# Kernel optimization log

Hardware: AMD Instinct MI355X
Metric: run time of the kernel (lower is better)

## Reference

```python
import jax, jax.numpy as jnp
import numpy as np

B, K, D = 4, 8192, 1024


def setup_inputs() -> dict:
    key = jax.random.key(0)
    kx, kw, kb = jax.random.split(key, 3)
    x = jax.random.normal(kx, (B, K, D), dtype=jnp.float32)
    # torch.nn.Linear default init: U(-1/sqrt(fan_in), 1/sqrt(fan_in))
    bound = 1.0 / np.sqrt(D)
    W = jax.random.uniform(kw, (D, D), dtype=jnp.float32, minval=-bound, maxval=bound)
    b = jax.random.uniform(kb, (D,), dtype=jnp.float32, minval=-bound, maxval=bound)
    return {"x": x, "W": W, "b": b}


def reference(x, W, b):
    # lam_t = sigmoid(x_t @ W^T + b): compute for all timesteps in one GEMM
    lam = jax.nn.sigmoid(jnp.einsum("bkd,ed->bke", x, W) + b)  # [B,K,D]
    u_gated = (1.0 - lam) * x  # [B,K,D]

    def step(s, inputs):
        lam_t, ug_t = inputs  # each [B,D]
        s = lam_t * s + ug_t
        return s, s

    s0 = jnp.zeros((x.shape[0], x.shape[2]), dtype=x.dtype)
    # scan over time axis: move K to leading dim
    _, ys = jax.lax.scan(step, s0, (jnp.swapaxes(lam, 0, 1), jnp.swapaxes(u_gated, 0, 1)))
    return jnp.swapaxes(ys, 0, 1)  # [B,K,D]
```

## Files before the change

kernel.cpp:

```cpp
#include <hip/hip_runtime.h>
#include <hip/hip_bf16.h>
#include <hip/hip_fp16.h>
#include <cstdint>
#include <cstddef>

#define B_ 4
#define K_ 8192
#define D_ 1024
#define M_ (B_*K_)
#define BD_ (B_*D_)

#define CCH 256
#define LCH (K_/CCH)

typedef __bf16    bf16x8 __attribute__((ext_vector_type(8)));
typedef float     f32x4  __attribute__((ext_vector_type(4)));
typedef _Float16  f16x4  __attribute__((ext_vector_type(4)));

typedef __attribute__((address_space(1))) void as1void;
typedef __attribute__((address_space(3))) void as3void;

__device__ __forceinline__ void gload_lds16(const void* g, void* l) {
  __builtin_amdgcn_global_load_lds((as1void*)g, (as3void*)l, 16, 0, 0);
}

__device__ __forceinline__ unsigned short f2bf_rne(float f) {
  unsigned u = __builtin_bit_cast(unsigned, f);
  u += 0x7fffu + ((u >> 16) & 1u);
  return (unsigned short)(u >> 16);
}

__global__ __launch_bounds__(256) void cvt_f32_to_bf16(
    const float* __restrict__ in, unsigned short* __restrict__ out, int n4) {
  int stride = gridDim.x * blockDim.x;
  for (int i = blockIdx.x * blockDim.x + threadIdx.x; i < n4; i += stride) {
    float4 v = reinterpret_cast<const float4*>(in)[i];
    ushort4 o;
    o.x = f2bf_rne(v.x); o.y = f2bf_rne(v.y);
    o.z = f2bf_rne(v.z); o.w = f2bf_rne(v.w);
    reinterpret_cast<ushort4*>(out)[i] = o;
  }
}

__global__ __launch_bounds__(256) void gemm_bias_sigmoid(
    const unsigned short* __restrict__ A,
    const unsigned short* __restrict__ Bw,
    const float* __restrict__ bias,
    _Float16* __restrict__ lamh) {
  __shared__ __attribute__((aligned(16))) unsigned short Alds[128 * 32];
  __shared__ __attribute__((aligned(16))) unsigned short Blds[128 * 32];

  const int t    = threadIdx.x;
  const int wave = t >> 6;
  const int lane = t & 63;
  const int wr   = wave >> 1;
  const int wc   = wave & 1;
  const int m0   = blockIdx.x * 128;
  const int n0   = blockIdx.y * 128;

  f32x4 acc[4][4] = {};

  const int r0 = t >> 2;
  const int c0 = (t & 3) * 8;
  const unsigned short* gA0 = A  + (size_t)(m0 + r0)      * D_ + c0;
  const unsigned short* gA1 = A  + (size_t)(m0 + r0 + 64) * D_ + c0;
  const unsigned short* gB0 = Bw + (size_t)(n0 + r0)      * D_ + c0;
  const unsigned short* gB1 = Bw + (size_t)(n0 + r0 + 64) * D_ + c0;
  unsigned short* lA0 = Alds + (       wave * 64) * 8;
  unsigned short* lA1 = Alds + (256 +  wave * 64) * 8;
  unsigned short* lB0 = Blds + (       wave * 64) * 8;
  unsigned short* lB1 = Blds + (256 +  wave * 64) * 8;

  const int aoff = (wr * 64 + (lane & 15)) * 32 + ((lane >> 4) * 8);
  const int boff = (wc * 64 + (lane & 15)) * 32 + ((lane >> 4) * 8);

  for (int kt = 0; kt < D_; kt += 32) {
    gload_lds16(gA0 + kt, lA0);
    gload_lds16(gA1 + kt, lA1);
    gload_lds16(gB0 + kt, lB0);
    gload_lds16(gB1 + kt, lB1);
    __syncthreads();
    bf16x8 af[4], bf[4];
#pragma unroll
    for (int m = 0; m < 4; ++m)
      af[m] = *reinterpret_cast<const bf16x8*>(&Alds[aoff + m * 16 * 32]);
#pragma unroll
    for (int n = 0; n < 4; ++n)
      bf[n] = *reinterpret_cast<const bf16x8*>(&Blds[boff + n * 16 * 32]);
#pragma unroll
    for (int m = 0; m < 4; ++m)
#pragma unroll
      for (int n = 0; n < 4; ++n)
        acc[m][n] = __builtin_amdgcn_mfma_f32_16x16x32_bf16(af[m], bf[n], acc[m][n], 0, 0, 0);
    __syncthreads();
  }

  const int erow = m0 + wr * 64 + ((lane >> 4) << 2);
  const int ecol = n0 + wc * 64 + (lane & 15);
#pragma unroll
  for (int n = 0; n < 4; ++n) {
    const int col = ecol + n * 16;
    const float bv = bias[col];
#pragma unroll
    for (int m = 0; m < 4; ++m) {
#pragma unroll
      for (int r = 0; r < 4; ++r) {
        const int row = erow + m * 16 + r;
        const float z = acc[m][n][r] + bv;
        lamh[(size_t)row * D_ + col] = (_Float16)(1.0f / (1.0f + __expf(-z)));
      }
    }
  }
}

__global__ __launch_bounds__(256) void scan_pass1(
    const _Float16* __restrict__ lamh, const float* __restrict__ x,
    float* __restrict__ P, float* __restrict__ Aarr) {
  const int blk = blockIdx.x;
  const int b = blk / CCH, c = blk % CCH;
  const int d4 = threadIdx.x * 4;
  const size_t base = ((size_t)(b * K_ + c * LCH)) * D_ + d4;
  const f16x4*  lp = reinterpret_cast<const f16x4*>(lamh + base);
  const float4* xp = reinterpret_cast<const float4*>(x + base);
  float4 s = {0.f, 0.f, 0.f, 0.f};
  float4 p = {1.f, 1.f, 1.f, 1.f};
#pragma unroll 8
  for (int k = 0; k < LCH; ++k) {
    f16x4  lh = lp[k * (D_ / 4)];
    float4 xv = xp[k * (D_ / 4)];
    float lx = (float)lh.x, ly = (float)lh.y, lz = (float)lh.z, lw = (float)lh.w;
    p.x *= lx; p.y *= ly; p.z *= lz; p.w *= lw;
    s.x = lx * s.x + (1.f - lx) * xv.x;
    s.y = ly * s.y + (1.f - ly) * xv.y;
    s.z = lz * s.z + (1.f - lz) * xv.z;
    s.w = lw * s.w + (1.f - lw) * xv.w;
  }
  const size_t o = (size_t)c * BD_ + b * D_ + d4;
  *reinterpret_cast<float4*>(P + o)    = p;
  *reinterpret_cast<float4*>(Aarr + o) = s;
}

__global__ __launch_bounds__(256) void scan_pass2(
    const float* __restrict__ P, const float* __restrict__ Aarr,
    float* __restrict__ S) {
  const int g = blockIdx.x * 256 + threadIdx.x;
  float s = 0.f;
  size_t o = g;
  for (int c0 = 0; c0 < CCH; c0 += 8) {
    float p[8], a[8];
#pragma unroll
    for (int j = 0; j < 8; ++j) {
      p[j] = P[o + (size_t)j * BD_];
      a[j] = Aarr[o + (size_t)j * BD_];
    }
    float sv[8];
#pragma unroll
    for (int j = 0; j < 8; ++j) {
      sv[j] = s;
      s = fmaf(p[j], s, a[j]);
    }
#pragma unroll
    for (int j = 0; j < 8; ++j)
      S[o + (size_t)j * BD_] = sv[j];
    o += (size_t)8 * BD_;
  }
}

__global__ __launch_bounds__(256) void scan_pass3(
    const _Float16* __restrict__ lamh, const float* __restrict__ x,
    const float* __restrict__ S, float* __restrict__ out) {
  const int blk = blockIdx.x;
  const int b = blk / CCH, c = blk % CCH;
  const int d4 = threadIdx.x * 4;
  float4 s = *reinterpret_cast<const float4*>(S + (size_t)c * BD_ + b * D_ + d4);
  const size_t base = ((size_t)(b * K_ + c * LCH)) * D_ + d4;
  const f16x4*  lp = reinterpret_cast<const f16x4*>(lamh + base);
  const float4* xp = reinterpret_cast<const float4*>(x + base);
  float4* op = reinterpret_cast<float4*>(out + base);
#pragma unroll 8
  for (int k = 0; k < LCH; ++k) {
    f16x4  lh = lp[k * (D_ / 4)];
    float4 xv = xp[k * (D_ / 4)];
    float lx = (float)lh.x, ly = (float)lh.y, lz = (float)lh.z, lw = (float)lh.w;
    s.x = lx * s.x + (1.f - lx) * xv.x;
    s.y = ly * s.y + (1.f - ly) * xv.y;
    s.z = lz * s.z + (1.f - lz) * xv.z;
    s.w = lw * s.w + (1.f - lw) * xv.w;
    op[k * (D_ / 4)] = s;
  }
}

extern "C" void kernel_launch(void* const* d_in, const int* in_sizes, int n_in,
                              void* d_out, int out_size, void* d_ws, size_t ws_size,
                              hipStream_t stream) {
  const float* x    = (const float*)d_in[0];
  const float* W    = (const float*)d_in[1];
  const float* bias = (const float*)d_in[2];
  float* out = (float*)d_out;

  char* ws = (char*)d_ws;
  unsigned short* xbf = (unsigned short*)ws;
  unsigned short* wbf = (unsigned short*)(ws + (size_t)M_ * D_ * 2);
  _Float16* lamh = (_Float16*)(ws + (size_t)M_ * D_ * 2 + (size_t)D_ * D_ * 2);
  float* P    = (float*)((char*)lamh + (size_t)M_ * D_ * 2);
  float* Aarr = P   + (size_t)CCH * BD_;
  float* S    = Aarr + (size_t)CCH * BD_;

  cvt_f32_to_bf16<<<2048, 256, 0, stream>>>(x, xbf, M_ * D_ / 4);
  cvt_f32_to_bf16<<<512, 256, 0, stream>>>(W, wbf, D_ * D_ / 4);
  gemm_bias_sigmoid<<<dim3(M_ / 128, D_ / 128), 256, 0, stream>>>(xbf, wbf, bias, lamh);
  scan_pass1<<<B_ * CCH, 256, 0, stream>>>(lamh, x, P, Aarr);
  scan_pass2<<<BD_ / 256, 256, 0, stream>>>(P, Aarr, S);
  scan_pass3<<<B_ * CCH, 256, 0, stream>>>(lamh, x, S, out);
}
```

Before: 438.8 us.

## Rewrite GEMM as 256x256 tile with 4-stage LDS pipeline and XCD swizzle

The GEMM moves from 128x128 tiles with a single synchronous LDS buffer to 256x256 tiles over 8 waves. It uses a 4-deep ring of global-to-LDS async loads gated by vmcnt waits, raises MFMA priority, and maps block IDs so that neighbouring row tiles share an XCD. The goal is to hide global load latency and raise arithmetic intensity. The scan chunk count is also doubled so pass1 and pass3 get more parallelism, at the cost of a longer serial pass2. The new layout needs 128KB of dynamic LDS per block, which limits occupancy, and it depends on hand-written waitcnt counts being correct.

```diff
diff --git a/kernel.cpp b/kernel.cpp
--- a/kernel.cpp
+++ b/kernel.cpp
@@ -10,8 +10,10 @@
 #define M_ (B_*K_)
 #define BD_ (B_*D_)
 
-#define CCH 256
+#define CCH 512
 #define LCH (K_/CCH)
+
+#define NTK 32
 
 typedef __bf16    bf16x8 __attribute__((ext_vector_type(8)));
 typedef float     f32x4  __attribute__((ext_vector_type(4)));
@@ -42,71 +44,88 @@
   }
 }
 
-__global__ __launch_bounds__(256) void gemm_bias_sigmoid(
+__global__ __launch_bounds__(512, 2) void gemm_bias_sigmoid(
     const unsigned short* __restrict__ A,
     const unsigned short* __restrict__ Bw,
     const float* __restrict__ bias,
     _Float16* __restrict__ lamh) {
-  __shared__ __attribute__((aligned(16))) unsigned short Alds[128 * 32];
-  __shared__ __attribute__((aligned(16))) unsigned short Blds[128 * 32];
+  extern __shared__ __attribute__((aligned(16))) unsigned short lds[];
 
   const int t    = threadIdx.x;
   const int wave = t >> 6;
   const int lane = t & 63;
-  const int wr   = wave >> 1;
-  const int wc   = wave & 1;
-  const int m0   = blockIdx.x * 128;
-  const int n0   = blockIdx.y * 128;
-
-  f32x4 acc[4][4] = {};
-
-  const int r0 = t >> 2;
-  const int c0 = (t & 3) * 8;
-  const unsigned short* gA0 = A  + (size_t)(m0 + r0)      * D_ + c0;
-  const unsigned short* gA1 = A  + (size_t)(m0 + r0 + 64) * D_ + c0;
-  const unsigned short* gB0 = Bw + (size_t)(n0 + r0)      * D_ + c0;
-  const unsigned short* gB1 = Bw + (size_t)(n0 + r0 + 64) * D_ + c0;
-  unsigned short* lA0 = Alds + (       wave * 64) * 8;
-  unsigned short* lA1 = Alds + (256 +  wave * 64) * 8;
-  unsigned short* lB0 = Blds + (       wave * 64) * 8;
-  unsigned short* lB1 = Blds + (256 +  wave * 64) * 8;
-
-  const int aoff = (wr * 64 + (lane & 15)) * 32 + ((lane >> 4) * 8);
-  const int boff = (wc * 64 + (lane & 15)) * 32 + ((lane >> 4) * 8);
-
-  for (int kt = 0; kt < D_; kt += 32) {
-    gload_lds16(gA0 + kt, lA0);
-    gload_lds16(gA1 + kt, lA1);
-    gload_lds16(gB0 + kt, lB0);
-    gload_lds16(gB1 + kt, lB1);
-    __syncthreads();
-    bf16x8 af[4], bf[4];
-#pragma unroll
-    for (int m = 0; m < 4; ++m)
-      af[m] = *reinterpret_cast<const bf16x8*>(&Alds[aoff + m * 16 * 32]);
-#pragma unroll
-    for (int n = 0; n < 4; ++n)
-      bf[n] = *reinterpret_cast<const bf16x8*>(&Blds[boff + n * 16 * 32]);
-#pragma unroll
-    for (int m = 0; m < 4; ++m)
-#pragma unroll
-      for (int n = 0; n < 4; ++n)
-        acc[m][n] = __builtin_amdgcn_mfma_f32_16x16x32_bf16(af[m], bf[n], acc[m][n], 0, 0, 0);
-    __syncthreads();
-  }
-
-  const int erow = m0 + wr * 64 + ((lane >> 4) << 2);
-  const int ecol = n0 + wc * 64 + (lane & 15);
-#pragma unroll
-  for (int n = 0; n < 4; ++n) {
-    const int col = ecol + n * 16;
+  const int wm   = wave >> 2;
+  const int wn   = wave & 3;
+
+  const int b     = blockIdx.x;
+  const int xcd   = b & 7;
+  const int inner = b >> 3;
+  const int cblk  = inner & 3;
+  const int rblk  = (inner >> 2) * 8 + xcd;
+  const int m0    = rblk * 256;
+  const int n0    = cblk * 256;
+
+  f32x4 acc[8][4] = {};
+
+  const int sg  = wave & 3;
+  const int rc0 = (wave >> 2) * 2;
+
+  auto STAGE = [&](int buf, int kt) {
+#pragma unroll
+    for (int i = 0; i < 2; ++i) {
+      const int rc = rc0 + i;
+      unsigned short* la = &lds[buf * 16384 + sg * 2048 + (rc * 64 + lane) * 8];
+      const unsigned short* ga = A + (size_t)(m0 + rc * 64 + lane) * D_ + kt + sg * 8;
+      gload_lds16(ga, la);
+      unsigned short* lb = la + 8192;
+      const unsigned short* gb = Bw + (size_t)(n0 + rc * 64 + lane) * D_ + kt + sg * 8;
+      gload_lds16(gb, lb);
+    }
+  };
+
+  const int rl = lane & 15, kg = lane >> 4;
+  const int aoff = kg * 2048 + rl * 8 + wm * 1024;
+  const int boff = kg * 2048 + rl * 8 + wn * 512 + 8192;
+
+  STAGE(0, 0); STAGE(1, 32); STAGE(2, 64);
+
+  for (int tt = 0; tt < NTK; ++tt) {
+    if (tt < NTK - 2)       asm volatile("s_waitcnt vmcnt(8)" ::: "memory");
+    else if (tt == NTK - 2) asm volatile("s_waitcnt vmcnt(4)" ::: "memory");
+    else                    asm volatile("s_waitcnt vmcnt(0)" ::: "memory");
+    __builtin_amdgcn_s_barrier();
+    asm volatile("" ::: "memory");
+    if (tt + 3 < NTK) STAGE((tt + 3) & 3, (tt + 3) * 32);
+    const int base = (tt & 3) * 16384;
+    bf16x8 af[8]; bf16x8 bfr[4];
+#pragma unroll
+    for (int mf = 0; mf < 8; ++mf)
+      af[mf] = *reinterpret_cast<const bf16x8*>(&lds[base + aoff + mf * 128]);
+#pragma unroll
+    for (int nf = 0; nf < 4; ++nf)
+      bfr[nf] = *reinterpret_cast<const bf16x8*>(&lds[base + boff + nf * 128]);
+    __builtin_amdgcn_s_setprio(1);
+#pragma unroll
+    for (int mf = 0; mf < 8; ++mf)
+#pragma unroll
+      for (int nf = 0; nf < 4; ++nf)
+        acc[mf][nf] = __builtin_amdgcn_mfma_f32_16x16x32_bf16(af[mf], bfr[nf], acc[mf][nf], 0, 0, 0);
+    __builtin_amdgcn_s_setprio(0);
+    asm volatile("" ::: "memory");
+  }
+
+  const int erow = m0 + wm * 128 + (lane >> 4) * 4;
+  const int ecol = n0 + wn * 64 + rl;
+#pragma unroll
+  for (int nf = 0; nf < 4; ++nf) {
+    const int col = ecol + nf * 16;
     const float bv = bias[col];
 #pragma unroll
-    for (int m = 0; m < 4; ++m) {
+    for (int mf = 0; mf < 8; ++mf) {
 #pragma unroll
       for (int r = 0; r < 4; ++r) {
-        const int row = erow + m * 16 + r;
-        const float z = acc[m][n][r] + bv;
+        const int row = erow + mf * 16 + r;
+        const float z = acc[mf][nf][r] + bv;
         lamh[(size_t)row * D_ + col] = (_Float16)(1.0f / (1.0f + __expf(-z)));
       }
     }
@@ -146,23 +165,23 @@
   const int g = blockIdx.x * 256 + threadIdx.x;
   float s = 0.f;
   size_t o = g;
-  for (int c0 = 0; c0 < CCH; c0 += 8) {
-    float p[8], a[8];
-#pragma unroll
-    for (int j = 0; j < 8; ++j) {
+  for (int c0 = 0; c0 < CCH; c0 += 16) {
+    float p[16], a[16];
+#pragma unroll
+    for (int j = 0; j < 16; ++j) {
       p[j] = P[o + (size_t)j * BD_];
       a[j] = Aarr[o + (size_t)j * BD_];
     }
-    float sv[8];
-#pragma unroll
-    for (int j = 0; j < 8; ++j) {
+    float sv[16];
+#pragma unroll
+    for (int j = 0; j < 16; ++j) {
       sv[j] = s;
       s = fmaf(p[j], s, a[j]);
     }
 #pragma unroll
-    for (int j = 0; j < 8; ++j)
+    for (int j = 0; j < 16; ++j)
       S[o + (size_t)j * BD_] = sv[j];
-    o += (size_t)8 * BD_;
+    o += (size_t)16 * BD_;
   }
 }
 
@@ -206,9 +225,12 @@
   float* Aarr = P   + (size_t)CCH * BD_;
   float* S    = Aarr + (size_t)CCH * BD_;
 
+  (void)hipFuncSetAttribute((const void*)gemm_bias_sigmoid,
+                            hipFuncAttributeMaxDynamicSharedMemorySize, 131072);
+
   cvt_f32_to_bf16<<<2048, 256, 0, stream>>>(x, xbf, M_ * D_ / 4);
   cvt_f32_to_bf16<<<512, 256, 0, stream>>>(W, wbf, D_ * D_ / 4);
-  gemm_bias_sigmoid<<<dim3(M_ / 128, D_ / 128), 256, 0, stream>>>(xbf, wbf, bias, lamh);
+  gemm_bias_sigmoid<<<512, 512, 131072, stream>>>(xbf, wbf, bias, lamh);
   scan_pass1<<<B_ * CCH, 256, 0, stream>>>(lamh, x, P, Aarr);
   scan_pass2<<<BD_ / 256, 256, 0, stream>>>(P, Aarr, S);
   scan_pass3<<<B_ * CCH, 256, 0, stream>>>(lamh, x, S, out);
```

Measured after the change: 439.8 us. About the same (+0.2%).
